# Kernel tuning notes

Hardware: AMD Instinct MI355X
Metric: run time of the kernel (lower is better)

The kernel has to match this reference:

```python
import jax, jax.numpy as jnp
import numpy as np

N_U = 20000; N_I = 20000; D = 256
NNZ = 600000; EGG = 300000; EDD = 300000; B = 8192
DROP = 0.1; LAM2 = 1e-7


def _attention(x, W, a, edges):
    # GAT-style attention over sampled relationship edges (src -> tgt).
    n, d = x.shape
    h = x @ W                                  # [n, d]
    src, tgt = edges[0], edges[1]
    e = jax.nn.leaky_relu((h @ a[:d])[src] + (h @ a[d:])[tgt], 0.2)  # [E]
    m = jax.ops.segment_max(e, tgt, num_segments=n)
    m = jnp.where(jnp.isfinite(m), m, 0.0)
    ex = jnp.exp(e - m[tgt])
    denom = jax.ops.segment_sum(ex, tgt, num_segments=n)             # [n]
    num = jax.ops.segment_sum(ex[:, None] * h[src], tgt, num_segments=n)  # [n, d]
    return num / (denom[:, None] + 1e-9)


def _spmm(rows, cols, vals, x, n_out):
    # sparse [n_out, n_in] @ dense [n_in, d]
    return jax.ops.segment_sum(vals[:, None] * x[cols], rows, num_segments=n_out)


def _mlp(x, W1, b1, W2, b2, W3, b3):
    h = jax.nn.relu(x @ W1 + b1)
    h = jax.nn.relu(h @ W2 + b2)
    return (h @ W3 + b3)[..., 0]


def setup_inputs() -> dict:
    key = jax.random.key(0)
    ks = jax.random.split(key, 24)
    s = 0.02
    inp = {
        'E_g_0': jax.random.normal(ks[0], (N_U, D), jnp.float32) * s,
        'E_d_0': jax.random.normal(ks[1], (N_I, D), jnp.float32) * s,
        'att_W': jax.random.normal(ks[2], (D, D), jnp.float32) * s,
        'att_a': jax.random.normal(ks[3], (2 * D,), jnp.float32) * s,
        'att1_W': jax.random.normal(ks[4], (D, D), jnp.float32) * s,
        'att1_a': jax.random.normal(ks[5], (2 * D,), jnp.float32) * s,
        'W1': jax.random.normal(ks[6], (2 * D, D), jnp.float32) * s,
        'b1': jnp.zeros((D,), jnp.float32),
        'W2': jax.random.normal(ks[7], (D, D), jnp.float32) * s,
        'b2': jnp.zeros((D,), jnp.float32),
        'W3': jax.random.normal(ks[8], (D, 1), jnp.float32) * s,
        'b3': jnp.zeros((1,), jnp.float32),
        'M1': jax.random.normal(ks[9], (2 * D, D), jnp.float32) * s,
        'mb1': jnp.zeros((D,), jnp.float32),
        'M2': jax.random.normal(ks[10], (D, D), jnp.float32) * s,
        'mb2': jnp.zeros((D,), jnp.float32),
        'adj_vals': jax.random.uniform(ks[11], (NNZ,), jnp.float32),
        'uids': jax.random.randint(ks[12], (B,), 0, N_U, jnp.int32),
        'iids': jax.random.randint(ks[13], (B,), 0, N_I, jnp.int32),
        'pos': jax.random.randint(ks[14], (B,), 0, N_I, jnp.int32),
        'neg': jax.random.randint(ks[15], (B,), 0, N_I, jnp.int32),
        'gene_edges': jax.random.randint(ks[16], (2, EGG), 0, N_U, jnp.int32),
        'drug_edges': jax.random.randint(ks[17], (2, EDD), 0, N_I, jnp.int32),
        'adj_rows': jax.random.randint(ks[18], (NNZ,), 0, N_U, jnp.int32),
        'adj_cols': jax.random.randint(ks[19], (NNZ,), 0, N_I, jnp.int32),
        'drop1': jax.random.bernoulli(ks[20], 1.0 - DROP, (NNZ,)),
        'drop2': jax.random.bernoulli(ks[21], 1.0 - DROP, (NNZ,)),
    }
    return inp


def reference(E_g_0, E_d_0, att_W, att_a, att1_W, att1_a, W1, b1, W2, b2, W3, b3,
              M1, mb1, M2, mb2, adj_vals, uids, iids, pos, neg,
              gene_edges, drug_edges, adj_rows, adj_cols, drop1, drop2):
    # Attention-modulated layer-0 embeddings
    E_d0 = 0.1 * _attention(E_d_0, att_W, att_a, drug_edges) + E_d_0
    E_g0 = 0.1 * _attention(E_g_0, att_W, att_a, gene_edges) + E_g_0

    # sparse_dropout + spmm (two independent dropout draws, as in the source)
    scale = 1.0 / (1.0 - DROP)
    v1 = adj_vals * drop1.astype(adj_vals.dtype) * scale
    v2 = adj_vals * drop2.astype(adj_vals.dtype) * scale
    E_g = _spmm(adj_rows, adj_cols, v1, E_d0, N_U)   # adj @ E_d0
    E_d = _spmm(adj_cols, adj_rows, v2, E_g0, N_I)   # adj.T @ E_g0

    u = E_g[uids]; p = E_d[pos]; ng = E_d[neg]
    pos_s = _mlp(jnp.concatenate([u, p], axis=-1), W1, b1, W2, b2, W3, b3)
    neg_s = _mlp(jnp.concatenate([u, ng], axis=-1), W1, b1, W2, b2, W3, b3)

    # BCE-with-logits (labels 1 for pos, 0 for neg) + BPR term
    loss_pos = jnp.mean(jax.nn.softplus(-pos_s))
    loss_neg = jnp.mean(jax.nn.softplus(neg_s))
    loss_bpr = jnp.mean(jax.nn.softplus(-(pos_s - neg_s)))
    loss_r = loss_pos + loss_neg + loss_bpr

    params = (E_g_0, E_d_0, att_W, att_a, att1_W, att1_a,
              W1, b1, W2, b2, W3, b3, M1, mb1, M2, mb2)
    loss_reg = LAM2 * sum(jnp.sum(p_ * p_) for p_ in params)

    loss = loss_reg + loss_r  # loss_s == 0
    return jnp.stack([loss, loss_r, jnp.zeros((), loss.dtype)])
```

## Files before the change

### kernel.cpp

```cpp
#include <hip/hip_runtime.h>
#include <math.h>

#define N_NODES 20000
#define D       256
#define NNZ     600000
#define NEDGE   300000
#define BATCH   8192
#define DROP_SCALE (1.0f/0.9f)
#define LAM2_F  1e-7f

#define M_PAD   20096
#define CSTRIDE 20032

#define C_ATT 56
#define C_ADJ 80

#define BINW 320
#define NBIN 63
#define TILE_E 2048
#define EPT 8
#define T_ATT ((NEDGE + TILE_E - 1) / TILE_E)
#define T_ADJ ((NNZ + TILE_E - 1) / TILE_E)
#define NBLK_P1 (2 * T_ATT + 2 * T_ADJ)
#define CAP_BIN_ATT 5376
#define CAP_BIN_ADJ 6144

#define FP8_SCALE 256.0f
#define VSCALE    58980.0f
#define INV_VSCALE (1.0f/58980.0f)

typedef unsigned short u16;
typedef unsigned char  u8;
typedef __attribute__((ext_vector_type(8))) short bf16x8;
typedef __attribute__((ext_vector_type(4))) float f32x4;
typedef __attribute__((ext_vector_type(2))) float f32x2;
typedef __attribute__((ext_vector_type(4))) u16   v4h;
typedef __attribute__((ext_vector_type(4))) unsigned v4u;

__device__ inline float wave_reduce(float v) {
    #pragma unroll
    for (int off = 32; off > 0; off >>= 1) v += __shfl_down(v, off, 64);
    return v;
}

__device__ inline float softplus_f(float x) {
    float r = log1pf(__expf(-fabsf(x)));
    return x > 0.f ? x + r : r;
}

__device__ inline u16 f2bf(float f) {
    unsigned u = __float_as_uint(f);
    unsigned r = u + 0x7fff + ((u >> 16) & 1);
    return (u16)(r >> 16);
}
__device__ inline float bf2f(u16 b) { return __uint_as_float(((unsigned)b) << 16); }

__device__ inline u16 f2h(float f) {
    _Float16 h = (_Float16)f;
    return __builtin_bit_cast(u16, h);
}
__device__ inline float h2f(u16 b) {
    return (float)__builtin_bit_cast(_Float16, b);
}

__device__ inline unsigned f32x4_to_fp8x4(float a, float b, float c, float d) {
    int r = 0;
    r = __builtin_amdgcn_cvt_pk_fp8_f32(a, b, r, false);
    r = __builtin_amdgcn_cvt_pk_fp8_f32(c, d, r, true);
    return (unsigned)r;
}
__device__ inline u8 f32_to_fp8(float a) {
    int r = __builtin_amdgcn_cvt_pk_fp8_f32(a, a, 0, false);
    return (u8)(r & 0xff);
}

__device__ inline void gld_lds16(const void* g, void* l) {
    __builtin_amdgcn_global_load_lds((const __attribute__((address_space(1))) void*)g,
                                     (__attribute__((address_space(3))) void*)l, 16, 0, 0);
}

__global__ __launch_bounds__(256) void init_kernel(const unsigned char* __restrict__ drop,
                                                   const int* __restrict__ uids, const int* __restrict__ pos,
                                                   const int* __restrict__ neg,
                                                   const float* __restrict__ att_W, const float* __restrict__ att_a,
                                                   float* __restrict__ wlv, float* __restrict__ wrv,
                                                   unsigned* __restrict__ bm2, unsigned* __restrict__ bm3,
                                                   unsigned int* __restrict__ flag) {
    if (blockIdx.x < 96) {
        int i = blockIdx.x * blockDim.x + threadIdx.x;
        if (i < BATCH) {
            int v = uids[i];
            atomicOr(&bm2[v >> 5], 1u << (v & 31));
        } else if (i < 2 * BATCH) {
            int v = pos[i - BATCH];
            atomicOr(&bm3[v >> 5], 1u << (v & 31));
        } else {
            int v = neg[i - 2 * BATCH];
            atomicOr(&bm3[v >> 5], 1u << (v & 31));
        }
    } else if (blockIdx.x == 96) {
        __shared__ int cnt_s;
        if (threadIdx.x == 0) cnt_s = 0;
        __syncthreads();
        int c = 0;
        for (int i = threadIdx.x; i < 1024; i += blockDim.x)
            if (drop[4*i + 1] != 0) c++;
        atomicAdd(&cnt_s, c);
        __syncthreads();
        if (threadIdx.x == 0) *flag = (cnt_s > 64) ? 1u : 0u;
    } else {
        int t = threadIdx.x;
        float s1 = 0.f, s2 = 0.f;
        for (int n = 0; n < D; n++) {
            float w = att_W[(size_t)t * D + n];
            s1 += w * att_a[n];
            s2 += w * att_a[D + n];
        }
        wlv[t] = s1; wrv[t] = s2;
    }
}

__global__ __launch_bounds__(256) void p1_kernel(
        const int* __restrict__ dtgt, const int* __restrict__ dsrc,
        const int* __restrict__ gtgt, const int* __restrict__ gsrc,
        const int* __restrict__ ar,   const int* __restrict__ ac,
        const float* __restrict__ vals,
        const void* __restrict__ drop1, const void* __restrict__ drop2,
        const unsigned int* __restrict__ flag,
        const unsigned* __restrict__ bm2, const unsigned* __restrict__ bm3,
        int* __restrict__ pcur, unsigned* __restrict__ attbin, uint2* __restrict__ adjbin) {
    __shared__ int hist[NBIN];
    __shared__ int basep[NBIN];
    for (int i = threadIdx.x; i < NBIN; i += 256) hist[i] = 0;
    __syncthreads();

    int b = blockIdx.x;
    int s, t0;
    if (b < T_ATT)               { s = 0; t0 = b; }
    else if (b < 2 * T_ATT)      { s = 1; t0 = b - T_ATT; }
    else if (b < 2*T_ATT + T_ADJ){ s = 2; t0 = b - 2 * T_ATT; }
    else                         { s = 3; t0 = b - 2 * T_ATT - T_ADJ; }
    int base = t0 * TILE_E;
    int regN = (s < 2) ? NEDGE : NNZ;

    int bins[EPT], rank[EPT];
    unsigned key[EPT], pay[EPT];
    float pv[EPT];

    if (s < 2) {
        const int* tgt = (s == 0) ? dtgt : gtgt;
        const int* src = (s == 0) ? dsrc : gsrc;
        #pragma unroll
        for (int e = 0; e < EPT; e++) {
            int idx = base + e * 256 + threadIdx.x;
            rank[e] = -1;
            if (idx < regN) {
                int k = __builtin_nontemporal_load(tgt + idx);
                int sv = __builtin_nontemporal_load(src + idx);
                key[e] = (unsigned)k; pay[e] = (unsigned)sv;
                bins[e] = k / BINW;
                rank[e] = atomicAdd(&hist[bins[e]], 1);
            }
        }
    } else {
        const unsigned int bf = *flag;
        const int* keyp = (s == 2) ? ar : ac;
        const int* othp = (s == 2) ? ac : ar;
        const void* drp = (s == 2) ? drop1 : drop2;
        const unsigned* bm = (s == 2) ? bm2 : bm3;
        #pragma unroll
        for (int e = 0; e < EPT; e++) {
            int idx = base + e * 256 + threadIdx.x;
            rank[e] = -1;
            if (idx < regN) {
                int k = __builtin_nontemporal_load(keyp + idx);
                if ((bm[k >> 5] >> (k & 31)) & 1) {
                    bool keep = bf ? (__builtin_nontemporal_load((const u8*)drp + idx) != 0)
                                   : (__builtin_nontemporal_load((const unsigned*)drp + idx) != 0);
                    if (keep) {
                        float v = __builtin_nontemporal_load(vals + idx) * DROP_SCALE;
                        int oth = __builtin_nontemporal_load(othp + idx);
                        key[e] = (unsigned)k; pay[e] = (unsigned)oth; pv[e] = v;
                        bins[e] = k / BINW;
                        rank[e] = atomicAdd(&hist[bins[e]], 1);
                    }
                }
            }
        }
    }
    __syncthreads();
    for (int i = threadIdx.x; i < NBIN; i += 256) {
        int h = hist[i];
        basep[i] = h ? atomicAdd(&pcur[s * NBIN + i], h) : 0;
    }
    __syncthreads();
    if (s < 2) {
        unsigned* seg = attbin + (size_t)s * NBIN * CAP_BIN_ATT;
        #pragma unroll
        for (int e = 0; e < EPT; e++) {
            if (rank[e] < 0) continue;
            int pos = basep[bins[e]] + rank[e];
            if (pos < CAP_BIN_ATT)
                seg[(size_t)bins[e] * CAP_BIN_ATT + pos] = key[e] | (pay[e] << 16);
        }
    } else {
        uint2* seg = adjbin + (size_t)(s - 2) * NBIN * CAP_BIN_ADJ;
        #pragma unroll
        for (int e = 0; e < EPT; e++) {
            if (rank[e] < 0) continue;
            int pos = basep[bins[e]] + rank[e];
            if (pos < CAP_BIN_ADJ) {
                uint2 pr; pr.x = key[e] | (pay[e] << 16); pr.y = __float_as_uint(pv[e]);
                seg[(size_t)bins[e] * CAP_BIN_ADJ + pos] = pr;
            }
        }
    }
}

__global__ __launch_bounds__(1024) void p2_kernel(
        const int* __restrict__ pcur, const unsigned* __restrict__ attbin,
        const uint2* __restrict__ adjbin,
        const float* __restrict__ hl_d, const float* __restrict__ hr_d,
        const float* __restrict__ hl_g, const float* __restrict__ hr_g,
        int* __restrict__ cnt, unsigned* __restrict__ srcs, unsigned* __restrict__ adj) {
    int s   = blockIdx.x / NBIN;
    int bin = blockIdx.x - s * NBIN;
    int nodeBase = bin * BINW;
    __shared__ int cur[BINW];
    for (int t = threadIdx.x; t < BINW; t += blockDim.x) cur[t] = 0;
    __syncthreads();
    if (s < 2) {
        int m = pcur[s * NBIN + bin]; if (m > CAP_BIN_ATT) m = CAP_BIN_ATT;
        const unsigned* seg = attbin + ((size_t)s * NBIN + bin) * CAP_BIN_ATT;
        const float* hl = (s == 0) ? hl_d : hl_g;
        const float* hr = (s == 0) ? hr_d : hr_g;
        for (int k = threadIdx.x; k < m; k += blockDim.x) {
            unsigned e = seg[k];
            int lk  = (int)(e & 0xFFFFu) - nodeBase;
            int src = (int)(e >> 16);
            float ev = hl[src] + hr[nodeBase + lk];
            ev = ev > 0.f ? ev : 0.2f * ev;
            u16 xh = f2h(__expf(ev));
            int c = atomicAdd(&cur[lk], 1);
            if (c < C_ATT)
                srcs[(size_t)s * N_NODES * C_ATT + (size_t)(nodeBase + lk) * C_ATT + c] =
                    (unsigned)src | ((unsigned)xh << 16);
        }
        __syncthreads();
        for (int t = threadIdx.x; t < BINW; t += blockDim.x) {
            int node = nodeBase + t;
            if (node < N_NODES) {
                int n = cur[t]; if (n > C_ATT) n = C_ATT;
                cnt[s * CSTRIDE + node] = n;
            }
        }
    } else {
        int m = pcur[s * NBIN + bin]; if (m > CAP_BIN_ADJ) m = CAP_BIN_ADJ;
        const uint2* seg = adjbin + ((size_t)(s - 2) * NBIN + bin) * CAP_BIN_ADJ;
        for (int k = threadIdx.x; k < m; k += blockDim.x) {
            uint2 e = seg[k];
            int lk  = (int)(e.x & 0xFFFFu) - nodeBase;
            int oth = (int)(e.x >> 16);
            float v = __uint_as_float(e.y);
            unsigned pk = ((unsigned)(v * VSCALE + 0.5f) << 16) | (unsigned)oth;
            int c = atomicAdd(&cur[lk], 1);
            if (c < C_ADJ)
                adj[(size_t)(s - 2) * N_NODES * C_ADJ + (size_t)(nodeBase + lk) * C_ADJ + c] = pk;
        }
        __syncthreads();
        for (int t = threadIdx.x; t < BINW; t += blockDim.x) {
            int node = nodeBase + t;
            if (node < N_NODES) {
                int n = cur[t]; if (n > C_ADJ) n = C_ADJ;
                cnt[s * CSTRIDE + node] = n;
            }
        }
    }
}

#define NB_CAST (2 * M_PAD / 4)
#define NB_T1   (D * D / 256)
#define NB_T2   (2 * D * D / 256)
#define NB_T3   (D * D / 256)
__global__ __launch_bounds__(256) void prep_kernel(
        const float* __restrict__ E_g, const float* __restrict__ E_d,
        u16* __restrict__ Eg_bf, u16* __restrict__ Ed_bf,
        const float* __restrict__ att_W,
        const float* __restrict__ W1, const float* __restrict__ W2,
        u16* __restrict__ attWT, u16* __restrict__ W1T, u16* __restrict__ W2T,
        const float* __restrict__ wlv, const float* __restrict__ wrv,
        float* __restrict__ hl_g, float* __restrict__ hr_g,
        float* __restrict__ hl_d, float* __restrict__ hr_d,
        float* __restrict__ regp) {
    int bid = blockIdx.x;
    if (bid < NB_CAST) {
        int wid  = (bid * 256 + threadIdx.x) >> 6;
        int lane = threadIdx.x & 63;
        int is_d = (wid >= M_PAD);
        int row  = is_d ? wid - M_PAD : wid;
        u16* dst = (is_d ? Ed_bf : Eg_bf) + (size_t)row * D;
        float s3 = 0.f;
        if (row >= N_NODES) {
            ((ushort4*)dst)[lane] = make_ushort4(0, 0, 0, 0);
        } else {
            const float* src = (is_d ? E_d : E_g) + (size_t)row * D;
            float4 e  = ((const float4*)src)[lane];
            float4 l4 = ((const float4*)wlv)[lane];
            float4 r4 = ((const float4*)wrv)[lane];
            ((ushort4*)dst)[lane] = make_ushort4(f2bf(e.x), f2bf(e.y), f2bf(e.z), f2bf(e.w));
            float s1 = e.x*l4.x + e.y*l4.y + e.z*l4.z + e.w*l4.w;
            float s2 = e.x*r4.x + e.y*r4.y + e.z*r4.z + e.w*r4.w;
            s3 = e.x*e.x + e.y*e.y + e.z*e.z + e.w*e.w;
            s1 = wave_reduce(s1); s2 = wave_reduce(s2);
            if (lane == 0) {
                if (is_d) { hl_d[row] = s1; hr_d[row] = s2; }
                else      { hl_g[row] = s1; hr_g[row] = s2; }
            }
        }
        s3 = wave_reduce(s3);
        __shared__ float sm3[4];
        if (lane == 0) sm3[threadIdx.x >> 6] = s3;
        __syncthreads();
        if (threadIdx.x == 0) regp[bid] = sm3[0] + sm3[1] + sm3[2] + sm3[3];
    } else if (bid < NB_CAST + NB_T1) {
        int o = (bid - NB_CAST) * 256 + threadIdx.x;
        int n = o >> 8, k = o & 255;
        attWT[o] = f2bf(att_W[(size_t)k * D + n]);
    } else if (bid < NB_CAST + NB_T1 + NB_T2) {
        int o = (bid - NB_CAST - NB_T1) * 256 + threadIdx.x;
        int n = o / (2 * D), k = o - n * (2 * D);
        W1T[o] = f2bf(W1[(size_t)k * D + n]);
    } else {
        int o = (bid - NB_CAST - NB_T1 - NB_T2) * 256 + threadIdx.x;
        int n = o >> 8, k = o & 255;
        W2T[o] = f2bf(W2[(size_t)k * D + n]);
    }
}

__global__ __launch_bounds__(256) void gemm_bf16(const u16* __restrict__ A_, const u16* __restrict__ BT,
                                                 void* __restrict__ C_, int M, int N, int K,
                                                 const float* __restrict__ bias, int do_relu, int out_mode,
                                                 const u16* __restrict__ A2, void* __restrict__ C2) {
    const u16* A = A_; void* C = C_;
    if (A2 && blockIdx.z == 1) { A = A2; C = C2; }
    __shared__ __align__(16) short As[128][32];
    __shared__ __align__(16) short Bs[128][32];
    int tid = threadIdx.x;
    int wave = tid >> 6, lane = tid & 63;
    int bm = blockIdx.x * 128, bn = blockIdx.y * 128;
    int sr = lane >> 2;
    int sc = (lane & 3) * 8;

    f32x4 acc[4][4];
    #pragma unroll
    for (int i = 0; i < 4; i++)
        #pragma unroll
        for (int j = 0; j < 4; j++)
            #pragma unroll
            for (int r = 0; r < 4; r++) acc[i][j][r] = 0.f;

    int wr = (wave >> 1) * 64;
    int wc = (wave & 1) * 64;
    int fr = lane & 15;
    int fk = (lane >> 4) * 8;

    for (int k0 = 0; k0 < K; k0 += 32) {
        #pragma unroll
        for (int j = 0; j < 2; j++) {
            int r0 = wave * 32 + j * 16;
            gld_lds16(A  + (size_t)(bm + r0 + sr) * K + k0 + sc, &As[r0][0]);
            gld_lds16(BT + (size_t)(bn + r0 + sr) * K + k0 + sc, &Bs[r0][0]);
        }
        __syncthreads();
        bf16x8 af[4], bfr[4];
        #pragma unroll
        for (int i = 0; i < 4; i++) af[i]  = *(const bf16x8*)&As[wr + i*16 + fr][fk];
        #pragma unroll
        for (int j = 0; j < 4; j++) bfr[j] = *(const bf16x8*)&Bs[wc + j*16 + fr][fk];
        #pragma unroll
        for (int i = 0; i < 4; i++)
            #pragma unroll
            for (int j = 0; j < 4; j++)
                acc[i][j] = __builtin_amdgcn_mfma_f32_16x16x32_bf16(af[i], bfr[j], acc[i][j], 0, 0, 0);
        __syncthreads();
    }

    #pragma unroll
    for (int j = 0; j < 4; j++) {
        int col = bn + wc + j * 16 + fr;
        float bv = (bias && out_mode == 0) ? bias[col] : 0.f;
        #pragma unroll
        for (int i = 0; i < 4; i++) {
            #pragma unroll
            for (int r = 0; r < 4; r++) {
                int row = bm + wr + i * 16 + (lane >> 4) * 4 + r;
                if (row < M) {
                    float v = acc[i][j][r] + bv;
                    if (out_mode == 0) {
                        if (do_relu) v = fmaxf(v, 0.f);
                        ((u16*)C)[(size_t)row * N + col] = f2bf(v);
                    } else {
                        ((u8*)C)[(size_t)row * N + col] = f32_to_fp8(v * FP8_SCALE);
                    }
                }
            }
        }
    }
}

__global__ __launch_bounds__(256) void att_kernel(const u8* __restrict__ h_d, const u8* __restrict__ h_g,
                                                  const int* __restrict__ cur, const unsigned* __restrict__ srcs,
                                                  const u16* __restrict__ Ed_bf, const u16* __restrict__ Eg_bf,
                                                  u8* __restrict__ E_d0p, u8* __restrict__ E_g0p) {
    int wid  = (blockIdx.x * blockDim.x + threadIdx.x) >> 6;
    int lane = threadIdx.x & 63;
    if (wid >= 2 * N_NODES) return;
    int is_g = (wid >= N_NODES);
    int node = is_g ? wid - N_NODES : wid;
    const unsigned* h32 = (const unsigned*)(is_g ? h_g : h_d);
    int reg = is_g ? 1 : 0;
    const unsigned* sv = srcs + (size_t)reg * N_NODES * C_ATT + (size_t)node * C_ATT;
    int n = cur[reg * CSTRIDE + node];
    if (n > C_ATT) n = C_ATT;
    float ax = 0.f, ay = 0.f, az = 0.f, aw = 0.f, denom = 0.f;
    int k = 0;
    for (; k + 8 <= n; k += 8) {
        v4u qa = __builtin_nontemporal_load((const v4u*)(sv + k));
        v4u qb = __builtin_nontemporal_load((const v4u*)(sv + k + 4));
        unsigned g[8]; float x[8];
        #pragma unroll
        for (int j = 0; j < 4; j++) {
            g[j]     = h32[((size_t)(qa[j] & 0xFFFFu) << 6) + lane];
            g[4 + j] = h32[((size_t)(qb[j] & 0xFFFFu) << 6) + lane];
            x[j]     = h2f((u16)(qa[j] >> 16));
            x[4 + j] = h2f((u16)(qb[j] >> 16));
        }
        #pragma unroll
        for (int j = 0; j < 8; j++) {
            denom += x[j];
            f32x2 lo = __builtin_amdgcn_cvt_pk_f32_fp8(g[j], false);
            f32x2 hi = __builtin_amdgcn_cvt_pk_f32_fp8(g[j], true);
            ax += x[j]*lo[0]; ay += x[j]*lo[1]; az += x[j]*hi[0]; aw += x[j]*hi[1];
        }
    }
    for (; k + 4 <= n; k += 4) {
        v4u qa = __builtin_nontemporal_load((const v4u*)(sv + k));
        unsigned g[4]; float x[4];
        #pragma unroll
        for (int j = 0; j < 4; j++) {
            g[j] = h32[((size_t)(qa[j] & 0xFFFFu) << 6) + lane];
            x[j] = h2f((u16)(qa[j] >> 16));
        }
        #pragma unroll
        for (int j = 0; j < 4; j++) {
            denom += x[j];
            f32x2 lo = __builtin_amdgcn_cvt_pk_f32_fp8(g[j], false);
            f32x2 hi = __builtin_amdgcn_cvt_pk_f32_fp8(g[j], true);
            ax += x[j]*lo[0]; ay += x[j]*lo[1]; az += x[j]*hi[0]; aw += x[j]*hi[1];
        }
    }
    for (; k < n; k++) {
        unsigned q = sv[k];
        float xv = h2f((u16)(q >> 16));
        unsigned g = h32[((size_t)(q & 0xFFFFu) << 6) + lane];
        denom += xv;
        f32x2 lo = __builtin_amdgcn_cvt_pk_f32_fp8(g, false);
        f32x2 hi = __builtin_amdgcn_cvt_pk_f32_fp8(g, true);
        ax += xv*lo[0]; ay += xv*lo[1]; az += xv*hi[0]; aw += xv*hi[1];
    }
    float sc = 0.1f / (denom + 1e-9f);
    const u16* E0b = is_g ? Eg_bf : Ed_bf;
    u8*       out  = is_g ? E_g0p : E_d0p;
    ushort4 b4 = ((const ushort4*)(E0b + (size_t)node * D))[lane];
    unsigned pk = f32x4_to_fp8x4(FP8_SCALE * bf2f(b4.x) + sc * ax, FP8_SCALE * bf2f(b4.y) + sc * ay,
                                 FP8_SCALE * bf2f(b4.z) + sc * az, FP8_SCALE * bf2f(b4.w) + sc * aw);
    ((unsigned*)(out + (size_t)node * D))[lane] = pk;
}

__global__ __launch_bounds__(256) void pull_kernel(const int* __restrict__ uids, const int* __restrict__ pos,
                                                   const int* __restrict__ neg,
                                                   const int* __restrict__ cur, const unsigned* __restrict__ adj,
                                                   const u8* __restrict__ E_d0p, const u8* __restrict__ E_g0p,
                                                   u16* __restrict__ X) {
    int wid  = (blockIdx.x * blockDim.x + threadIdx.x) >> 6;
    int lane = threadIdx.x & 63;
    if (wid >= 3 * BATCH) return;
    int type = wid >> 13;
    int b    = wid & (BATCH - 1);
    int node, reg; const u8* E;
    if (type == 0)      { node = uids[b]; reg = 2; E = E_d0p; }
    else if (type == 1) { node = pos[b];  reg = 3; E = E_g0p; }
    else                { node = neg[b];  reg = 3; E = E_g0p; }
    const unsigned* E32 = (const unsigned*)E;
    const unsigned* av = adj + (size_t)(reg - 2) * N_NODES * C_ADJ + (size_t)node * C_ADJ;
    int n = cur[reg * CSTRIDE + node];
    if (n > C_ADJ) n = C_ADJ;
    float ax = 0.f, ay = 0.f, az = 0.f, aw = 0.f;
    int k = 0;
    for (; k + 8 <= n; k += 8) {
        v4u qa = __builtin_nontemporal_load((const v4u*)(av + k));
        v4u qb = __builtin_nontemporal_load((const v4u*)(av + k + 4));
        unsigned g[8]; float v[8];
        #pragma unroll
        for (int j = 0; j < 4; j++) {
            g[j]     = E32[((size_t)(qa[j] & 0xFFFFu) << 6) + lane];
            g[4 + j] = E32[((size_t)(qb[j] & 0xFFFFu) << 6) + lane];
            v[j]     = (float)(qa[j] >> 16) * INV_VSCALE;
            v[4 + j] = (float)(qb[j] >> 16) * INV_VSCALE;
        }
        #pragma unroll
        for (int j = 0; j < 8; j++) {
            f32x2 lo = __builtin_amdgcn_cvt_pk_f32_fp8(g[j], false);
            f32x2 hi = __builtin_amdgcn_cvt_pk_f32_fp8(g[j], true);
            ax += v[j]*lo[0]; ay += v[j]*lo[1]; az += v[j]*hi[0]; aw += v[j]*hi[1];
        }
    }
    for (; k + 4 <= n; k += 4) {
        v4u qa = __builtin_nontemporal_load((const v4u*)(av + k));
        unsigned g[4]; float v[4];
        #pragma unroll
        for (int j = 0; j < 4; j++) {
            g[j] = E32[((size_t)(qa[j] & 0xFFFFu) << 6) + lane];
            v[j] = (float)(qa[j] >> 16) * INV_VSCALE;
        }
        #pragma unroll
        for (int j = 0; j < 4; j++) {
            f32x2 lo = __builtin_amdgcn_cvt_pk_f32_fp8(g[j], false);
            f32x2 hi = __builtin_amdgcn_cvt_pk_f32_fp8(g[j], true);
            ax += v[j]*lo[0]; ay += v[j]*lo[1]; az += v[j]*hi[0]; aw += v[j]*hi[1];
        }
    }
    for (; k < n; k++) {
        unsigned q = av[k];
        int c = q & 0xFFFF;
        float v = (float)(q >> 16) * INV_VSCALE;
        unsigned g = E32[((size_t)c << 6) + lane];
        f32x2 lo = __builtin_amdgcn_cvt_pk_f32_fp8(g, false);
        f32x2 hi = __builtin_amdgcn_cvt_pk_f32_fp8(g, true);
        ax += v*lo[0]; ay += v*lo[1]; az += v*hi[0]; aw += v*hi[1];
    }
    const float inv = 1.0f / FP8_SCALE;
    ushort4 r = make_ushort4(f2bf(ax * inv), f2bf(ay * inv), f2bf(az * inv), f2bf(aw * inv));
    if (type == 0) {
        ((ushort4*)(X + (size_t)b * 2 * D))[lane] = r;
        ((ushort4*)(X + (size_t)(BATCH + b) * 2 * D))[lane] = r;
    } else if (type == 1) {
        ((ushort4*)(X + (size_t)b * 2 * D + D))[lane] = r;
    } else {
        ((ushort4*)(X + (size_t)(BATCH + b) * 2 * D + D))[lane] = r;
    }
}

__global__ __launch_bounds__(256) void score_kernel(const u16* __restrict__ H2, const float* __restrict__ W3,
                                                    const float* __restrict__ b3, float* __restrict__ s) {
    int wid  = (blockIdx.x * blockDim.x + threadIdx.x) >> 6;
    int lane = threadIdx.x & 63;
    if (wid >= 2 * BATCH) return;
    ushort4 hv = ((const ushort4*)(H2 + (size_t)wid * D))[lane];
    float4 w  = ((const float4*)W3)[lane];
    float d = bf2f(hv.x) * w.x + bf2f(hv.y) * w.y + bf2f(hv.z) * w.z + bf2f(hv.w) * w.w;
    d = wave_reduce(d);
    if (lane == 0) s[wid] = d + b3[0];
}

__global__ __launch_bounds__(256) void loss_kernel(const float* __restrict__ s, float* __restrict__ acc) {
    float lp = 0.f, ln = 0.f, lb = 0.f;
    for (int i = blockIdx.x * blockDim.x + threadIdx.x; i < BATCH; i += gridDim.x * blockDim.x) {
        float ps = s[i], ns = s[BATCH + i];
        lp += softplus_f(-ps);
        ln += softplus_f(ns);
        lb += softplus_f(-(ps - ns));
    }
    lp = wave_reduce(lp); ln = wave_reduce(ln); lb = wave_reduce(lb);
    __shared__ float sm[3][4];
    int w = threadIdx.x >> 6, lane = threadIdx.x & 63;
    if (lane == 0) { sm[0][w] = lp; sm[1][w] = ln; sm[2][w] = lb; }
    __syncthreads();
    if (threadIdx.x == 0) {
        float a = 0.f, b = 0.f, c = 0.f;
        for (int i = 0; i < 4; i++) { a += sm[0][i]; b += sm[1][i]; c += sm[2][i]; }
        atomicAdd(&acc[1], a); atomicAdd(&acc[2], b); atomicAdd(&acc[3], c);
    }
}

struct RegArgs { const float* p[14]; int n[14]; };

__global__ __launch_bounds__(256) void reg_kernel(RegArgs ra, float* __restrict__ acc) {
    const float* p = ra.p[blockIdx.x];
    int n = ra.n[blockIdx.x];
    int base = blockIdx.y * 4096;
    if (base >= n) return;
    float sum = 0.f;
    if (base + 4096 <= n) {
        const float4* p4 = (const float4*)(p + base);
        float4 v = p4[threadIdx.x];
        sum += v.x*v.x + v.y*v.y + v.z*v.z + v.w*v.w;
        v = p4[256 + threadIdx.x];
        sum += v.x*v.x + v.y*v.y + v.z*v.z + v.w*v.w;
        v = p4[512 + threadIdx.x];
        sum += v.x*v.x + v.y*v.y + v.z*v.z + v.w*v.w;
        v = p4[768 + threadIdx.x];
        sum += v.x*v.x + v.y*v.y + v.z*v.z + v.w*v.w;
    } else {
        int end = n;
        for (int i = base + threadIdx.x; i < end; i += 256) { float v = p[i]; sum += v * v; }
    }
    sum = wave_reduce(sum);
    __shared__ float sm[4];
    int w = threadIdx.x >> 6, lane = threadIdx.x & 63;
    if (lane == 0) sm[w] = sum;
    __syncthreads();
    if (threadIdx.x == 0) atomicAdd(&acc[0], sm[0] + sm[1] + sm[2] + sm[3]);
}

__global__ __launch_bounds__(256) void final_kernel(const float* __restrict__ acc,
                                                    const float* __restrict__ regp,
                                                    float* __restrict__ out) {
    float sum = 0.f;
    for (int i = threadIdx.x; i < NB_CAST; i += 256) sum += regp[i];
    sum = wave_reduce(sum);
    __shared__ float sm[4];
    int w = threadIdx.x >> 6, lane = threadIdx.x & 63;
    if (lane == 0) sm[w] = sum;
    __syncthreads();
    if (threadIdx.x == 0) {
        float reg = acc[0] + sm[0] + sm[1] + sm[2] + sm[3];
        float lr = (acc[1] + acc[2] + acc[3]) * (1.0f / (float)BATCH);
        out[0] = LAM2_F * reg + lr;
        out[1] = lr;
        out[2] = 0.f;
    }
}

extern "C" void kernel_launch(void* const* d_in, const int* in_sizes, int n_in,
                              void* d_out, int out_size, void* d_ws, size_t ws_size,
                              hipStream_t stream) {
    (void)n_in; (void)out_size; (void)ws_size;
    const float* E_g_0   = (const float*)d_in[0];
    const float* E_d_0   = (const float*)d_in[1];
    const float* att_W   = (const float*)d_in[2];
    const float* att_a   = (const float*)d_in[3];
    const float* W1      = (const float*)d_in[6];
    const float* b1      = (const float*)d_in[7];
    const float* W2      = (const float*)d_in[8];
    const float* b2      = (const float*)d_in[9];
    const float* W3      = (const float*)d_in[10];
    const float* b3      = (const float*)d_in[11];
    const float* adj_vals= (const float*)d_in[16];
    const int*   uids    = (const int*)d_in[17];
    const int*   pos     = (const int*)d_in[19];
    const int*   neg     = (const int*)d_in[20];
    const int*   gene_e  = (const int*)d_in[21];
    const int*   drug_e  = (const int*)d_in[22];
    const int*   adj_rows= (const int*)d_in[23];
    const int*   adj_cols= (const int*)d_in[24];
    const void*  drop1   = d_in[25];
    const void*  drop2   = d_in[26];

    char* ws = (char*)d_ws;
    size_t cur_off = 0;
    auto take = [&](size_t bytes) -> void* {
        void* p = ws + cur_off;
        cur_off += (bytes + 255) & ~(size_t)255;
        return p;
    };
    u16* Eg_bf = (u16*)take((size_t)M_PAD * D * 2);
    u16* Ed_bf = (u16*)take((size_t)M_PAD * D * 2);
    u16* X     = Eg_bf;
    u16* attWT = (u16*)take((size_t)D * D * 2);
    u16* W1T   = (u16*)take((size_t)D * 2 * D * 2);
    u16* W2T   = (u16*)take((size_t)D * D * 2);
    u8*  h_g   = (u8*)take((size_t)M_PAD * D);
    u8*  h_d   = (u8*)take((size_t)M_PAD * D);
    u8*  E_g0p = (u8*)take((size_t)N_NODES * D);
    u8*  E_d0p = (u8*)take((size_t)N_NODES * D);
    u16* H1    = (u16*)take((size_t)2 * BATCH * D * 2);
    u16* H2    = (u16*)take((size_t)2 * BATCH * D * 2);
    float* hl_g = (float*)take((size_t)N_NODES * 4);
    float* hr_g = (float*)take((size_t)N_NODES * 4);
    float* hl_d = (float*)take((size_t)N_NODES * 4);
    float* hr_d = (float*)take((size_t)N_NODES * 4);
    float* wlv  = (float*)take((size_t)D * 4);
    float* wrv  = (float*)take((size_t)D * 4);
    float* sbuf = (float*)take((size_t)2 * BATCH * 4);
    float* regp = (float*)take((size_t)NB_CAST * 4);
    unsigned* srcs = (unsigned*)take((size_t)2 * N_NODES * C_ATT * 4);
    unsigned* adj  = (unsigned*)take((size_t)2 * N_NODES * C_ADJ * 4);
    int*   cnt  = (int*)take((size_t)4 * CSTRIDE * 4);
    unsigned* attbin = (unsigned*)take((size_t)2 * NBIN * CAP_BIN_ATT * 4);
    uint2*    adjbin = (uint2*)take((size_t)2 * NBIN * CAP_BIN_ADJ * 8);
    int*      pcur = (int*)take((size_t)4 * NBIN * 4);
    unsigned* bm2  = (unsigned*)take(4096);
    unsigned* bm3  = (unsigned*)take(4096);
    float*    acc  = (float*)take(256);
    size_t zbytes = (char*)(acc + 64) - (char*)pcur;

    hipMemsetAsync(pcur, 0, zbytes, stream);
    init_kernel<<<98, 256, 0, stream>>>((const unsigned char*)drop1, uids, pos, neg,
                                        att_W, att_a, wlv, wrv,
                                        bm2, bm3, (unsigned int*)(acc + 4));

    p1_kernel<<<NBLK_P1, 256, 0, stream>>>(drug_e + NEDGE, drug_e, gene_e + NEDGE, gene_e,
                                           adj_rows, adj_cols, adj_vals, drop1, drop2,
                                           (const unsigned int*)(acc + 4), bm2, bm3,
                                           pcur, attbin, adjbin);

    prep_kernel<<<NB_CAST + NB_T1 + NB_T2 + NB_T3, 256, 0, stream>>>(
        E_g_0, E_d_0, Eg_bf, Ed_bf, att_W, W1, W2,
        attWT, W1T, W2T, wlv, wrv, hl_g, hr_g, hl_d, hr_d, regp);

    p2_kernel<<<4 * NBIN, 1024, 0, stream>>>(pcur, attbin, adjbin,
                                             hl_d, hr_d, hl_g, hr_g, cnt, srcs, adj);

    gemm_bf16<<<dim3(M_PAD / 128, 2, 2), 256, 0, stream>>>(Eg_bf, attWT, h_g, N_NODES, D, D,
                                                           nullptr, 0, 1, Ed_bf, h_d);
    att_kernel<<<10000, 256, 0, stream>>>(h_d, h_g, cnt, srcs,
                                          Ed_bf, Eg_bf, E_d0p, E_g0p);

    pull_kernel<<<6144, 256, 0, stream>>>(uids, pos, neg, cnt, adj, E_d0p, E_g0p, X);

    gemm_bf16<<<dim3(2 * BATCH / 128, 2, 1), 256, 0, stream>>>(X,  W1T, H1, 2 * BATCH, D, 2 * D,
                                                               b1, 1, 0, nullptr, nullptr);
    gemm_bf16<<<dim3(2 * BATCH / 128, 2, 1), 256, 0, stream>>>(H1, W2T, H2, 2 * BATCH, D, D,
                                                               b2, 1, 0, nullptr, nullptr);
    score_kernel<<<4096, 256, 0, stream>>>(H2, W3, b3, sbuf);

    loss_kernel<<<16, 256, 0, stream>>>(sbuf, acc);
    RegArgs ra;
    for (int i = 0; i < 14; i++) { ra.p[i] = (const float*)d_in[i + 2]; ra.n[i] = in_sizes[i + 2]; }
    reg_kernel<<<dim3(14, 32), 256, 0, stream>>>(ra, acc);
    final_kernel<<<1, 256, 0, stream>>>(acc, regp, (float*)d_out);
}
```

Measured before the change: 341.2 us.

## Fuse p1 with prep, score into second MLP GEMM, and loss/reg/final into one tail

Merges the binning kernel and the prep/cast kernel into one launch so their independent blocks run together. The second MLP GEMM now applies bias, ReLU and the W3 dot product in its epilogue and atomically accumulates scores into sbuf, which removes the H2 buffer and the score kernel. Loss, regularization and final reduction become a single tail kernel that uses a last-block counter. Each fusion cuts launches and memory traffic, at the cost of float atomics on the scores (order-dependent rounding) and a zeroed sbuf that the memset must now cover.

After: 326.5 us. 4.3% less time.

```diff
diff --git a/kernel.cpp b/kernel.cpp
--- a/kernel.cpp
+++ b/kernel.cpp
@@ -120,7 +120,12 @@
     }
 }
 
-__global__ __launch_bounds__(256) void p1_kernel(
+#define NB_CAST (2 * M_PAD / 4)
+#define NB_T1   (D * D / 256)
+#define NB_T2   (2 * D * D / 256)
+#define NB_T3   (D * D / 256)
+#define NB_PREP (NB_CAST + NB_T1 + NB_T2 + NB_T3)
+__global__ __launch_bounds__(256) void p1prep_kernel(
         const int* __restrict__ dtgt, const int* __restrict__ dsrc,
         const int* __restrict__ gtgt, const int* __restrict__ gsrc,
         const int* __restrict__ ar,   const int* __restrict__ ac,
@@ -128,91 +133,146 @@
         const void* __restrict__ drop1, const void* __restrict__ drop2,
         const unsigned int* __restrict__ flag,
         const unsigned* __restrict__ bm2, const unsigned* __restrict__ bm3,
-        int* __restrict__ pcur, unsigned* __restrict__ attbin, uint2* __restrict__ adjbin) {
-    __shared__ int hist[NBIN];
-    __shared__ int basep[NBIN];
-    for (int i = threadIdx.x; i < NBIN; i += 256) hist[i] = 0;
-    __syncthreads();
-
-    int b = blockIdx.x;
-    int s, t0;
-    if (b < T_ATT)               { s = 0; t0 = b; }
-    else if (b < 2 * T_ATT)      { s = 1; t0 = b - T_ATT; }
-    else if (b < 2*T_ATT + T_ADJ){ s = 2; t0 = b - 2 * T_ATT; }
-    else                         { s = 3; t0 = b - 2 * T_ATT - T_ADJ; }
-    int base = t0 * TILE_E;
-    int regN = (s < 2) ? NEDGE : NNZ;
-
-    int bins[EPT], rank[EPT];
-    unsigned key[EPT], pay[EPT];
-    float pv[EPT];
-
-    if (s < 2) {
-        const int* tgt = (s == 0) ? dtgt : gtgt;
-        const int* src = (s == 0) ? dsrc : gsrc;
-        #pragma unroll
-        for (int e = 0; e < EPT; e++) {
-            int idx = base + e * 256 + threadIdx.x;
-            rank[e] = -1;
-            if (idx < regN) {
-                int k = __builtin_nontemporal_load(tgt + idx);
-                int sv = __builtin_nontemporal_load(src + idx);
-                key[e] = (unsigned)k; pay[e] = (unsigned)sv;
-                bins[e] = k / BINW;
-                rank[e] = atomicAdd(&hist[bins[e]], 1);
-            }
-        }
-    } else {
-        const unsigned int bf = *flag;
-        const int* keyp = (s == 2) ? ar : ac;
-        const int* othp = (s == 2) ? ac : ar;
-        const void* drp = (s == 2) ? drop1 : drop2;
-        const unsigned* bm = (s == 2) ? bm2 : bm3;
-        #pragma unroll
-        for (int e = 0; e < EPT; e++) {
-            int idx = base + e * 256 + threadIdx.x;
-            rank[e] = -1;
-            if (idx < regN) {
-                int k = __builtin_nontemporal_load(keyp + idx);
-                if ((bm[k >> 5] >> (k & 31)) & 1) {
-                    bool keep = bf ? (__builtin_nontemporal_load((const u8*)drp + idx) != 0)
-                                   : (__builtin_nontemporal_load((const unsigned*)drp + idx) != 0);
-                    if (keep) {
-                        float v = __builtin_nontemporal_load(vals + idx) * DROP_SCALE;
-                        int oth = __builtin_nontemporal_load(othp + idx);
-                        key[e] = (unsigned)k; pay[e] = (unsigned)oth; pv[e] = v;
-                        bins[e] = k / BINW;
-                        rank[e] = atomicAdd(&hist[bins[e]], 1);
+        int* __restrict__ pcur, unsigned* __restrict__ attbin, uint2* __restrict__ adjbin,
+        const float* __restrict__ E_g, const float* __restrict__ E_d,
+        u16* __restrict__ Eg_bf, u16* __restrict__ Ed_bf,
+        const float* __restrict__ att_W,
+        const float* __restrict__ W1, const float* __restrict__ W2,
+        u16* __restrict__ attWT, u16* __restrict__ W1T, u16* __restrict__ W2T,
+        const float* __restrict__ wlv, const float* __restrict__ wrv,
+        float* __restrict__ hl_g, float* __restrict__ hr_g,
+        float* __restrict__ hl_d, float* __restrict__ hr_d,
+        float* __restrict__ regp) {
+    if (blockIdx.x < NBLK_P1) {
+        __shared__ int hist[NBIN];
+        __shared__ int basep[NBIN];
+        for (int i = threadIdx.x; i < NBIN; i += 256) hist[i] = 0;
+        __syncthreads();
+
+        int b = blockIdx.x;
+        int s, t0;
+        if (b < T_ATT)               { s = 0; t0 = b; }
+        else if (b < 2 * T_ATT)      { s = 1; t0 = b - T_ATT; }
+        else if (b < 2*T_ATT + T_ADJ){ s = 2; t0 = b - 2 * T_ATT; }
+        else                         { s = 3; t0 = b - 2 * T_ATT - T_ADJ; }
+        int base = t0 * TILE_E;
+        int regN = (s < 2) ? NEDGE : NNZ;
+
+        int bins[EPT], rank[EPT];
+        unsigned key[EPT], pay[EPT];
+        float pv[EPT];
+
+        if (s < 2) {
+            const int* tgt = (s == 0) ? dtgt : gtgt;
+            const int* src = (s == 0) ? dsrc : gsrc;
+            #pragma unroll
+            for (int e = 0; e < EPT; e++) {
+                int idx = base + e * 256 + threadIdx.x;
+                rank[e] = -1;
+                if (idx < regN) {
+                    int k = __builtin_nontemporal_load(tgt + idx);
+                    int sv = __builtin_nontemporal_load(src + idx);
+                    key[e] = (unsigned)k; pay[e] = (unsigned)sv;
+                    bins[e] = k / BINW;
+                    rank[e] = atomicAdd(&hist[bins[e]], 1);
+                }
+            }
+        } else {
+            const unsigned int bf = *flag;
+            const int* keyp = (s == 2) ? ar : ac;
+            const int* othp = (s == 2) ? ac : ar;
+            const void* drp = (s == 2) ? drop1 : drop2;
+            const unsigned* bm = (s == 2) ? bm2 : bm3;
+            #pragma unroll
+            for (int e = 0; e < EPT; e++) {
+                int idx = base + e * 256 + threadIdx.x;
+                rank[e] = -1;
+                if (idx < regN) {
+                    int k = __builtin_nontemporal_load(keyp + idx);
+                    if ((bm[k >> 5] >> (k & 31)) & 1) {
+                        bool keep = bf ? (__builtin_nontemporal_load((const u8*)drp + idx) != 0)
+                                       : (__builtin_nontemporal_load((const unsigned*)drp + idx) != 0);
+                        if (keep) {
+                            float v = __builtin_nontemporal_load(vals + idx) * DROP_SCALE;
+                            int oth = __builtin_nontemporal_load(othp + idx);
+                            key[e] = (unsigned)k; pay[e] = (unsigned)oth; pv[e] = v;
+                            bins[e] = k / BINW;
+                            rank[e] = atomicAdd(&hist[bins[e]], 1);
+                        }
                     }
                 }
             }
         }
-    }
-    __syncthreads();
-    for (int i = threadIdx.x; i < NBIN; i += 256) {
-        int h = hist[i];
-        basep[i] = h ? atomicAdd(&pcur[s * NBIN + i], h) : 0;
-    }
-    __syncthreads();
-    if (s < 2) {
-        unsigned* seg = attbin + (size_t)s * NBIN * CAP_BIN_ATT;
-        #pragma unroll
-        for (int e = 0; e < EPT; e++) {
-            if (rank[e] < 0) continue;
-            int pos = basep[bins[e]] + rank[e];
-            if (pos < CAP_BIN_ATT)
-                seg[(size_t)bins[e] * CAP_BIN_ATT + pos] = key[e] | (pay[e] << 16);
+        __syncthreads();
+        for (int i = threadIdx.x; i < NBIN; i += 256) {
+            int h = hist[i];
+            basep[i] = h ? atomicAdd(&pcur[s * NBIN + i], h) : 0;
+        }
+        __syncthreads();
+        if (s < 2) {
+            unsigned* seg = attbin + (size_t)s * NBIN * CAP_BIN_ATT;
+            #pragma unroll
+            for (int e = 0; e < EPT; e++) {
+                if (rank[e] < 0) continue;
+                int pos = basep[bins[e]] + rank[e];
+                if (pos < CAP_BIN_ATT)
+                    seg[(size_t)bins[e] * CAP_BIN_ATT + pos] = key[e] | (pay[e] << 16);
+            }
+        } else {
+            uint2* seg = adjbin + (size_t)(s - 2) * NBIN * CAP_BIN_ADJ;
+            #pragma unroll
+            for (int e = 0; e < EPT; e++) {
+                if (rank[e] < 0) continue;
+                int pos = basep[bins[e]] + rank[e];
+                if (pos < CAP_BIN_ADJ) {
+                    uint2 pr; pr.x = key[e] | (pay[e] << 16); pr.y = __float_as_uint(pv[e]);
+                    seg[(size_t)bins[e] * CAP_BIN_ADJ + pos] = pr;
+                }
+            }
         }
     } else {
-        uint2* seg = adjbin + (size_t)(s - 2) * NBIN * CAP_BIN_ADJ;
-        #pragma unroll
-        for (int e = 0; e < EPT; e++) {
-            if (rank[e] < 0) continue;
-            int pos = basep[bins[e]] + rank[e];
-            if (pos < CAP_BIN_ADJ) {
-                uint2 pr; pr.x = key[e] | (pay[e] << 16); pr.y = __float_as_uint(pv[e]);
-                seg[(size_t)bins[e] * CAP_BIN_ADJ + pos] = pr;
-            }
+        int bid = blockIdx.x - NBLK_P1;
+        if (bid < NB_CAST) {
+            int wid  = (bid * 256 + threadIdx.x) >> 6;
+            int lane = threadIdx.x & 63;
+            int is_d = (wid >= M_PAD);
+            int row  = is_d ? wid - M_PAD : wid;
+            u16* dst = (is_d ? Ed_bf : Eg_bf) + (size_t)row * D;
+            float s3 = 0.f;
+            if (row >= N_NODES) {
+                ((ushort4*)dst)[lane] = make_ushort4(0, 0, 0, 0);
+            } else {
+                const float* src = (is_d ? E_d : E_g) + (size_t)row * D;
+                float4 e  = ((const float4*)src)[lane];
+                float4 l4 = ((const float4*)wlv)[lane];
+                float4 r4 = ((const float4*)wrv)[lane];
+                ((ushort4*)dst)[lane] = make_ushort4(f2bf(e.x), f2bf(e.y), f2bf(e.z), f2bf(e.w));
+                float s1 = e.x*l4.x + e.y*l4.y + e.z*l4.z + e.w*l4.w;
+                float s2 = e.x*r4.x + e.y*r4.y + e.z*r4.z + e.w*r4.w;
+                s3 = e.x*e.x + e.y*e.y + e.z*e.z + e.w*e.w;
+                s1 = wave_reduce(s1); s2 = wave_reduce(s2);
+                if (lane == 0) {
+                    if (is_d) { hl_d[row] = s1; hr_d[row] = s2; }
+                    else      { hl_g[row] = s1; hr_g[row] = s2; }
+                }
+            }
+            s3 = wave_reduce(s3);
+            __shared__ float sm3[4];
+            if (lane == 0) sm3[threadIdx.x >> 6] = s3;
+            __syncthreads();
+            if (threadIdx.x == 0) regp[bid] = sm3[0] + sm3[1] + sm3[2] + sm3[3];
+        } else if (bid < NB_CAST + NB_T1) {
+            int o = (bid - NB_CAST) * 256 + threadIdx.x;
+            int n = o >> 8, k = o & 255;
+            attWT[o] = f2bf(att_W[(size_t)k * D + n]);
+        } else if (bid < NB_CAST + NB_T1 + NB_T2) {
+            int o = (bid - NB_CAST - NB_T1) * 256 + threadIdx.x;
+            int n = o / (2 * D), k = o - n * (2 * D);
+            W1T[o] = f2bf(W1[(size_t)k * D + n]);
+        } else {
+            int o = (bid - NB_CAST - NB_T1 - NB_T2) * 256 + threadIdx.x;
+            int n = o >> 8, k = o & 255;
+            W2T[o] = f2bf(W2[(size_t)k * D + n]);
         }
     }
 }
@@ -278,69 +338,11 @@
     }
 }
 
-#define NB_CAST (2 * M_PAD / 4)
-#define NB_T1   (D * D / 256)
-#define NB_T2   (2 * D * D / 256)
-#define NB_T3   (D * D / 256)
-__global__ __launch_bounds__(256) void prep_kernel(
-        const float* __restrict__ E_g, const float* __restrict__ E_d,
-        u16* __restrict__ Eg_bf, u16* __restrict__ Ed_bf,
-        const float* __restrict__ att_W,
-        const float* __restrict__ W1, const float* __restrict__ W2,
-        u16* __restrict__ attWT, u16* __restrict__ W1T, u16* __restrict__ W2T,
-        const float* __restrict__ wlv, const float* __restrict__ wrv,
-        float* __restrict__ hl_g, float* __restrict__ hr_g,
-        float* __restrict__ hl_d, float* __restrict__ hr_d,
-        float* __restrict__ regp) {
-    int bid = blockIdx.x;
-    if (bid < NB_CAST) {
-        int wid  = (bid * 256 + threadIdx.x) >> 6;
-        int lane = threadIdx.x & 63;
-        int is_d = (wid >= M_PAD);
-        int row  = is_d ? wid - M_PAD : wid;
-        u16* dst = (is_d ? Ed_bf : Eg_bf) + (size_t)row * D;
-        float s3 = 0.f;
-        if (row >= N_NODES) {
-            ((ushort4*)dst)[lane] = make_ushort4(0, 0, 0, 0);
-        } else {
-            const float* src = (is_d ? E_d : E_g) + (size_t)row * D;
-            float4 e  = ((const float4*)src)[lane];
-            float4 l4 = ((const float4*)wlv)[lane];
-            float4 r4 = ((const float4*)wrv)[lane];
-            ((ushort4*)dst)[lane] = make_ushort4(f2bf(e.x), f2bf(e.y), f2bf(e.z), f2bf(e.w));
-            float s1 = e.x*l4.x + e.y*l4.y + e.z*l4.z + e.w*l4.w;
-            float s2 = e.x*r4.x + e.y*r4.y + e.z*r4.z + e.w*r4.w;
-            s3 = e.x*e.x + e.y*e.y + e.z*e.z + e.w*e.w;
-            s1 = wave_reduce(s1); s2 = wave_reduce(s2);
-            if (lane == 0) {
-                if (is_d) { hl_d[row] = s1; hr_d[row] = s2; }
-                else      { hl_g[row] = s1; hr_g[row] = s2; }
-            }
-        }
-        s3 = wave_reduce(s3);
-        __shared__ float sm3[4];
-        if (lane == 0) sm3[threadIdx.x >> 6] = s3;
-        __syncthreads();
-        if (threadIdx.x == 0) regp[bid] = sm3[0] + sm3[1] + sm3[2] + sm3[3];
-    } else if (bid < NB_CAST + NB_T1) {
-        int o = (bid - NB_CAST) * 256 + threadIdx.x;
-        int n = o >> 8, k = o & 255;
-        attWT[o] = f2bf(att_W[(size_t)k * D + n]);
-    } else if (bid < NB_CAST + NB_T1 + NB_T2) {
-        int o = (bid - NB_CAST - NB_T1) * 256 + threadIdx.x;
-        int n = o / (2 * D), k = o - n * (2 * D);
-        W1T[o] = f2bf(W1[(size_t)k * D + n]);
-    } else {
-        int o = (bid - NB_CAST - NB_T1 - NB_T2) * 256 + threadIdx.x;
-        int n = o >> 8, k = o & 255;
-        W2T[o] = f2bf(W2[(size_t)k * D + n]);
-    }
-}
-
 __global__ __launch_bounds__(256) void gemm_bf16(const u16* __restrict__ A_, const u16* __restrict__ BT,
                                                  void* __restrict__ C_, int M, int N, int K,
                                                  const float* __restrict__ bias, int do_relu, int out_mode,
-                                                 const u16* __restrict__ A2, void* __restrict__ C2) {
+                                                 const u16* __restrict__ A2, void* __restrict__ C2,
+                                                 const float* __restrict__ w3) {
     const u16* A = A_; void* C = C_;
     if (A2 && blockIdx.z == 1) { A = A2; C = C2; }
     __shared__ __align__(16) short As[128][32];
@@ -383,6 +385,42 @@
             for (int j = 0; j < 4; j++)
                 acc[i][j] = __builtin_amdgcn_mfma_f32_16x16x32_bf16(af[i], bfr[j], acc[i][j], 0, 0, 0);
         __syncthreads();
+    }
+
+    if (out_mode == 2) {
+        __shared__ float sacc[128];
+        for (int t = tid; t < 128; t += 256) sacc[t] = 0.f;
+        __syncthreads();
+        float bvj[4], w3j[4];
+        #pragma unroll
+        for (int j = 0; j < 4; j++) {
+            int col = bn + wc + j * 16 + fr;
+            bvj[j] = bias[col];
+            w3j[j] = w3[col];
+        }
+        #pragma unroll
+        for (int i = 0; i < 4; i++) {
+            #pragma unroll
+            for (int r = 0; r < 4; r++) {
+                float rs = 0.f;
+                #pragma unroll
+                for (int j = 0; j < 4; j++) {
+                    float v = fmaxf(acc[i][j][r] + bvj[j], 0.f);
+                    rs += v * w3j[j];
+                }
+                rs += __shfl_xor(rs, 1, 64);
+                rs += __shfl_xor(rs, 2, 64);
+                rs += __shfl_xor(rs, 4, 64);
+                rs += __shfl_xor(rs, 8, 64);
+                if (fr == 0)
+                    atomicAdd(&sacc[wr + i * 16 + (lane >> 4) * 4 + r], rs);
+            }
+        }
+        __syncthreads();
+        float* sb = (float*)C;
+        for (int t = tid; t < 128; t += 256)
+            atomicAdd(&sb[bm + t], sacc[t]);
+        return;
     }
 
     #pragma unroll
@@ -551,81 +589,83 @@
     }
 }
 
-__global__ __launch_bounds__(256) void score_kernel(const u16* __restrict__ H2, const float* __restrict__ W3,
-                                                    const float* __restrict__ b3, float* __restrict__ s) {
-    int wid  = (blockIdx.x * blockDim.x + threadIdx.x) >> 6;
-    int lane = threadIdx.x & 63;
-    if (wid >= 2 * BATCH) return;
-    ushort4 hv = ((const ushort4*)(H2 + (size_t)wid * D))[lane];
-    float4 w  = ((const float4*)W3)[lane];
-    float d = bf2f(hv.x) * w.x + bf2f(hv.y) * w.y + bf2f(hv.z) * w.z + bf2f(hv.w) * w.w;
-    d = wave_reduce(d);
-    if (lane == 0) s[wid] = d + b3[0];
-}
-
-__global__ __launch_bounds__(256) void loss_kernel(const float* __restrict__ s, float* __restrict__ acc) {
-    float lp = 0.f, ln = 0.f, lb = 0.f;
-    for (int i = blockIdx.x * blockDim.x + threadIdx.x; i < BATCH; i += gridDim.x * blockDim.x) {
-        float ps = s[i], ns = s[BATCH + i];
-        lp += softplus_f(-ps);
-        ln += softplus_f(ns);
-        lb += softplus_f(-(ps - ns));
-    }
-    lp = wave_reduce(lp); ln = wave_reduce(ln); lb = wave_reduce(lb);
+struct RegArgs { const float* p[14]; int n[14]; };
+#define NB_REG  448
+#define NB_LOSS 16
+#define NB_TAIL (NB_REG + NB_LOSS)
+
+__global__ __launch_bounds__(256) void tail_kernel(RegArgs ra, const float* __restrict__ s,
+                                                   const float* __restrict__ b3p,
+                                                   const float* __restrict__ regp,
+                                                   float* __restrict__ acc, float* __restrict__ out) {
+    int bid = blockIdx.x;
+    int w = threadIdx.x >> 6, lane = threadIdx.x & 63;
     __shared__ float sm[3][4];
-    int w = threadIdx.x >> 6, lane = threadIdx.x & 63;
-    if (lane == 0) { sm[0][w] = lp; sm[1][w] = ln; sm[2][w] = lb; }
+    __shared__ int lastf;
+    if (bid < NB_REG) {
+        const float* p = ra.p[bid >> 5];
+        int n = ra.n[bid >> 5];
+        int base = (bid & 31) * 4096;
+        if (base < n) {
+            float sum = 0.f;
+            if (base + 4096 <= n) {
+                const float4* p4 = (const float4*)(p + base);
+                float4 v = p4[threadIdx.x];
+                sum += v.x*v.x + v.y*v.y + v.z*v.z + v.w*v.w;
+                v = p4[256 + threadIdx.x];
+                sum += v.x*v.x + v.y*v.y + v.z*v.z + v.w*v.w;
+                v = p4[512 + threadIdx.x];
+                sum += v.x*v.x + v.y*v.y + v.z*v.z + v.w*v.w;
+                v = p4[768 + threadIdx.x];
+                sum += v.x*v.x + v.y*v.y + v.z*v.z + v.w*v.w;
+            } else {
+                for (int i = base + threadIdx.x; i < n; i += 256) { float v = p[i]; sum += v * v; }
+            }
+            sum = wave_reduce(sum);
+            if (lane == 0) sm[0][w] = sum;
+            __syncthreads();
+            if (threadIdx.x == 0)
+                atomicAdd(&acc[0], sm[0][0] + sm[0][1] + sm[0][2] + sm[0][3]);
+        }
+    } else {
+        float b3 = b3p[0];
+        float lp = 0.f, ln = 0.f, lb = 0.f;
+        for (int i = (bid - NB_REG) * 256 + threadIdx.x; i < BATCH; i += NB_LOSS * 256) {
+            float ps = s[i] + b3, ns = s[BATCH + i] + b3;
+            lp += softplus_f(-ps);
+            ln += softplus_f(ns);
+            lb += softplus_f(-(ps - ns));
+        }
+        lp = wave_reduce(lp); ln = wave_reduce(ln); lb = wave_reduce(lb);
+        if (lane == 0) { sm[0][w] = lp; sm[1][w] = ln; sm[2][w] = lb; }
+        __syncthreads();
+        if (threadIdx.x == 0) {
+            float a = 0.f, b = 0.f, c = 0.f;
+            for (int i = 0; i < 4; i++) { a += sm[0][i]; b += sm[1][i]; c += sm[2][i]; }
+            atomicAdd(&acc[1], a); atomicAdd(&acc[2], b); atomicAdd(&acc[3], c);
+        }
+    }
     __syncthreads();
     if (threadIdx.x == 0) {
-        float a = 0.f, b = 0.f, c = 0.f;
-        for (int i = 0; i < 4; i++) { a += sm[0][i]; b += sm[1][i]; c += sm[2][i]; }
-        atomicAdd(&acc[1], a); atomicAdd(&acc[2], b); atomicAdd(&acc[3], c);
-    }
-}
-
-struct RegArgs { const float* p[14]; int n[14]; };
-
-__global__ __launch_bounds__(256) void reg_kernel(RegArgs ra, float* __restrict__ acc) {
-    const float* p = ra.p[blockIdx.x];
-    int n = ra.n[blockIdx.x];
-    int base = blockIdx.y * 4096;
-    if (base >= n) return;
-    float sum = 0.f;
-    if (base + 4096 <= n) {
-        const float4* p4 = (const float4*)(p + base);
-        float4 v = p4[threadIdx.x];
-        sum += v.x*v.x + v.y*v.y + v.z*v.z + v.w*v.w;
-        v = p4[256 + threadIdx.x];
-        sum += v.x*v.x + v.y*v.y + v.z*v.z + v.w*v.w;
-        v = p4[512 + threadIdx.x];
-        sum += v.x*v.x + v.y*v.y + v.z*v.z + v.w*v.w;
-        v = p4[768 + threadIdx.x];
-        sum += v.x*v.x + v.y*v.y + v.z*v.z + v.w*v.w;
-    } else {
-        int end = n;
-        for (int i = base + threadIdx.x; i < end; i += 256) { float v = p[i]; sum += v * v; }
-    }
-    sum = wave_reduce(sum);
-    __shared__ float sm[4];
-    int w = threadIdx.x >> 6, lane = threadIdx.x & 63;
-    if (lane == 0) sm[w] = sum;
+        __threadfence();
+        unsigned t = atomicAdd((unsigned*)&acc[8], 1u);
+        lastf = (t == NB_TAIL - 1);
+    }
     __syncthreads();
-    if (threadIdx.x == 0) atomicAdd(&acc[0], sm[0] + sm[1] + sm[2] + sm[3]);
-}
-
-__global__ __launch_bounds__(256) void final_kernel(const float* __restrict__ acc,
-                                                    const float* __restrict__ regp,
-                                                    float* __restrict__ out) {
+    if (!lastf) return;
     float sum = 0.f;
     for (int i = threadIdx.x; i < NB_CAST; i += 256) sum += regp[i];
     sum = wave_reduce(sum);
-    __shared__ float sm[4];
-    int w = threadIdx.x >> 6, lane = threadIdx.x & 63;
-    if (lane == 0) sm[w] = sum;
+    if (lane == 0) sm[0][w] = sum;
     __syncthreads();
     if (threadIdx.x == 0) {
-        float reg = acc[0] + sm[0] + sm[1] + sm[2] + sm[3];
-        float lr = (acc[1] + acc[2] + acc[3]) * (1.0f / (float)BATCH);
+        __threadfence();
+        float a0 = atomicAdd(&acc[0], 0.f);
+        float a1 = atomicAdd(&acc[1], 0.f);
+        float a2 = atomicAdd(&acc[2], 0.f);
+        float a3 = atomicAdd(&acc[3], 0.f);
+        float reg = a0 + sm[0][0] + sm[0][1] + sm[0][2] + sm[0][3];
+        float lr = (a1 + a2 + a3) * (1.0f / (float)BATCH);
         out[0] = LAM2_F * reg + lr;
         out[1] = lr;
         out[2] = 0.f;
@@ -675,14 +715,12 @@
     u8*  E_g0p = (u8*)take((size_t)N_NODES * D);
     u8*  E_d0p = (u8*)take((size_t)N_NODES * D);
     u16* H1    = (u16*)take((size_t)2 * BATCH * D * 2);
-    u16* H2    = (u16*)take((size_t)2 * BATCH * D * 2);
     float* hl_g = (float*)take((size_t)N_NODES * 4);
     float* hr_g = (float*)take((size_t)N_NODES * 4);
     float* hl_d = (float*)take((size_t)N_NODES * 4);
     float* hr_d = (float*)take((size_t)N_NODES * 4);
     float* wlv  = (float*)take((size_t)D * 4);
     float* wrv  = (float*)take((size_t)D * 4);
-    float* sbuf = (float*)take((size_t)2 * BATCH * 4);
     float* regp = (float*)take((size_t)NB_CAST * 4);
     unsigned* srcs = (unsigned*)take((size_t)2 * N_NODES * C_ATT * 4);
     unsigned* adj  = (unsigned*)take((size_t)2 * N_NODES * C_ADJ * 4);
@@ -693,19 +731,19 @@
     unsigned* bm2  = (unsigned*)take(4096);
     unsigned* bm3  = (unsigned*)take(4096);
     float*    acc  = (float*)take(256);
-    size_t zbytes = (char*)(acc + 64) - (char*)pcur;
+    float*    sbuf = (float*)take((size_t)2 * BATCH * 4);
+    size_t zbytes = (char*)sbuf + (size_t)2 * BATCH * 4 - (char*)pcur;
 
     hipMemsetAsync(pcur, 0, zbytes, stream);
     init_kernel<<<98, 256, 0, stream>>>((const unsigned char*)drop1, uids, pos, neg,
                                         att_W, att_a, wlv, wrv,
                                         bm2, bm3, (unsigned int*)(acc + 4));
 
-    p1_kernel<<<NBLK_P1, 256, 0, stream>>>(drug_e + NEDGE, drug_e, gene_e + NEDGE, gene_e,
-                                           adj_rows, adj_cols, adj_vals, drop1, drop2,
-                                           (const unsigned int*)(acc + 4), bm2, bm3,
-                                           pcur, attbin, adjbin);
-
-    prep_kernel<<<NB_CAST + NB_T1 + NB_T2 + NB_T3, 256, 0, stream>>>(
+    p1prep_kernel<<<NBLK_P1 + NB_PREP, 256, 0, stream>>>(
+        drug_e + NEDGE, drug_e, gene_e + NEDGE, gene_e,
+        adj_rows, adj_cols, adj_vals, drop1, drop2,
+        (const unsigned int*)(acc + 4), bm2, bm3,
+        pcur, attbin, adjbin,
         E_g_0, E_d_0, Eg_bf, Ed_bf, att_W, W1, W2,
         attWT, W1T, W2T, wlv, wrv, hl_g, hr_g, hl_d, hr_d, regp);
 
@@ -713,21 +751,18 @@
                                              hl_d, hr_d, hl_g, hr_g, cnt, srcs, adj);
 
     gemm_bf16<<<dim3(M_PAD / 128, 2, 2), 256, 0, stream>>>(Eg_bf, attWT, h_g, N_NODES, D, D,
-                                                           nullptr, 0, 1, Ed_bf, h_d);
+                                                           nullptr, 0, 1, Ed_bf, h_d, nullptr);
     att_kernel<<<10000, 256, 0, stream>>>(h_d, h_g, cnt, srcs,
                                           Ed_bf, Eg_bf, E_d0p, E_g0p);
 
     pull_kernel<<<6144, 256, 0, stream>>>(uids, pos, neg, cnt, adj, E_d0p, E_g0p, X);
 
     gemm_bf16<<<dim3(2 * BATCH / 128, 2, 1), 256, 0, stream>>>(X,  W1T, H1, 2 * BATCH, D, 2 * D,
-                                                               b1, 1, 0, nullptr, nullptr);
-    gemm_bf16<<<dim3(2 * BATCH / 128, 2, 1), 256, 0, stream>>>(H1, W2T, H2, 2 * BATCH, D, D,
-                                                               b2, 1, 0, nullptr, nullptr);
-    score_kernel<<<4096, 256, 0, stream>>>(H2, W3, b3, sbuf);
-
-    loss_kernel<<<16, 256, 0, stream>>>(sbuf, acc);
+                                                               b1, 1, 0, nullptr, nullptr, nullptr);
+    gemm_bf16<<<dim3(2 * BATCH / 128, 2, 1), 256, 0, stream>>>(H1, W2T, sbuf, 2 * BATCH, D, D,
+                                                               b2, 1, 2, nullptr, nullptr, W3);
+
     RegArgs ra;
     for (int i = 0; i < 14; i++) { ra.p[i] = (const float*)d_in[i + 2]; ra.n[i] = in_sizes[i + 2]; }
-    reg_kernel<<<dim3(14, 32), 256, 0, stream>>>(ra, acc);
-    final_kernel<<<1, 256, 0, stream>>>(acc, regp, (float*)d_out);
-}
+    tail_kernel<<<NB_TAIL, 256, 0, stream>>>(ra, sbuf, b3, regp, acc, (float*)d_out);
+}
```
